# Kernel tuning notes

Measured on AMD Instinct MI355X. Metric: run time of the kernel, lower is better.

## Reference

```python
import jax, jax.numpy as jnp
import numpy as np

B, N, ND, H = 8, 1024, 64, 128
NUM_OPS, NUM_PARAMS, SKETCH = 64, 256, 128


def setup_inputs() -> dict:
    key = jax.random.key(0)
    ks = iter(jax.random.split(key, 64))

    def rn(shape, s=0.05):
        return jax.random.normal(next(ks), shape, dtype=jnp.float32) * s

    inp = {
        'node_features': jax.random.normal(next(ks), (B, N, ND), dtype=jnp.float32),
        'adjacency': (jax.random.uniform(next(ks), (B, N, N)) < 0.05).astype(jnp.float32),
        'mask': jnp.ones((B, N), jnp.float32),
    }
    for name, din in (('g1', ND), ('g2', H), ('g3', H)):
        inp[name + '_W'] = rn((din, H))
        inp[name + '_b'] = jnp.zeros((H,), jnp.float32)
        inp[name + '_aW'] = rn((2 * H,))
        inp[name + '_ab'] = jnp.zeros((), jnp.float32)
    for l in (0, 1):
        inp[f'l{l}_Wih'] = rn((4 * H, H))
        inp[f'l{l}_Whh'] = rn((4 * H, H))
        inp[f'l{l}_bih'] = jnp.zeros((4 * H,), jnp.float32)
        inp[f'l{l}_bhh'] = jnp.zeros((4 * H,), jnp.float32)
    for name, dout in (('op', NUM_OPS), ('pa', NUM_PARAMS), ('sk', SKETCH), ('no', ND)):
        inp[name + '_W1'] = rn((H, H))
        inp[name + '_b1'] = jnp.zeros((H,), jnp.float32)
        inp[name + '_W2'] = rn((H, dout))
        inp[name + '_b2'] = jnp.zeros((dout,), jnp.float32)
    return inp


def _gnn(x, adj, W, b, aW, ab):
    # h = Linear(x); att[b,i,j] = sigmoid(aW . [h_j ; h_i] + ab)  (cat order from the torch code)
    h = x @ W + b                      # [B,N,H]
    D = W.shape[1]
    sj = h @ aW[:D]                    # contribution of the dim-1-expanded term (h_j)
    si = h @ aW[D:]                    # contribution of the dim-2-expanded term (h_i)
    att = jax.nn.sigmoid(si[:, :, None] + sj[:, None, :] + ab) * adj  # [B,N,N]
    return jnp.einsum('bij,bjd->bid', att, h)


def _lstm(x, Wih, Whh, bih, bhh):
    # single torch-style LSTM layer, gate order i,f,g,o; zero initial state
    Bx, Hh = x.shape[0], Whh.shape[1]

    def step(carry, xt):
        h, c = carry
        g = xt @ Wih.T + h @ Whh.T + (bih + bhh)       # [B,4H]
        i, f, gg, o = jnp.split(g, 4, axis=-1)
        c = jax.nn.sigmoid(f) * c + jax.nn.sigmoid(i) * jnp.tanh(gg)
        h = jax.nn.sigmoid(o) * jnp.tanh(c)
        return (h, c), h

    z = jnp.zeros((Bx, Hh), x.dtype)
    _, ys = jax.lax.scan(step, (z, z), jnp.swapaxes(x, 0, 1))
    return jnp.swapaxes(ys, 0, 1)


def _mlp(x, W1, b1, W2, b2):
    return jax.nn.relu(x @ W1 + b1) @ W2 + b2


def reference(node_features, adjacency, mask,
              g1_W, g1_b, g1_aW, g1_ab,
              g2_W, g2_b, g2_aW, g2_ab,
              g3_W, g3_b, g3_aW, g3_ab,
              l0_Wih, l0_Whh, l0_bih, l0_bhh,
              l1_Wih, l1_Whh, l1_bih, l1_bhh,
              op_W1, op_b1, op_W2, op_b2,
              pa_W1, pa_b1, pa_W2, pa_b2,
              sk_W1, sk_b1, sk_W2, sk_b2,
              no_W1, no_b1, no_W2, no_b2):
    h = jax.nn.relu(_gnn(node_features, adjacency, g1_W, g1_b, g1_aW, g1_ab))
    h = jax.nn.relu(_gnn(h, adjacency, g2_W, g2_b, g2_aW, g2_ab))
    h = _gnn(h, adjacency, g3_W, g3_b, g3_aW, g3_ab)
    lo = _lstm(h, l0_Wih, l0_Whh, l0_bih, l0_bhh)
    lo = _lstm(lo, l1_Wih, l1_Whh, l1_bih, l1_bhh)
    op_pred = _mlp(lo, op_W1, op_b1, op_W2, op_b2)
    param_pred = _mlp(lo, pa_W1, pa_b1, pa_W2, pa_b2)
    sketch_pred = _mlp(lo, sk_W1, sk_b1, sk_W2, sk_b2)
    node_pred = _mlp(h, no_W1, no_b1, no_W2, no_b2)
    return (op_pred, param_pred, sketch_pred, node_pred)
```

## Files before the change

### kernel.cpp

```cpp
#include <hip/hip_runtime.h>
#include <hip/hip_fp16.h>

typedef __attribute__((ext_vector_type(8))) short short8;
typedef __attribute__((ext_vector_type(4))) float f32x4;
typedef __attribute__((ext_vector_type(2))) unsigned int u32x2;

__device__ __forceinline__ unsigned short bf16_of(float f) {
    unsigned u = __builtin_bit_cast(unsigned, f);
    u += 0x7fffu + ((u >> 16) & 1u);
    return (unsigned short)(u >> 16);
}
__device__ __forceinline__ unsigned bf16pk(float a, float b) {
    return (unsigned)bf16_of(a) | ((unsigned)bf16_of(b) << 16);
}
__device__ __forceinline__ unsigned fp16pk(float a, float b) {
    return __builtin_bit_cast(unsigned, __builtin_amdgcn_cvt_pkrtz(a, b));
}
__device__ __forceinline__ f32x4 h4f(u32x2 v) {
    __half2 a = __builtin_bit_cast(__half2, v[0]);
    __half2 b = __builtin_bit_cast(__half2, v[1]);
    float2 fa = __half22float2(a), fb = __half22float2(b);
    f32x4 r; r[0] = fa.x; r[1] = fa.y; r[2] = fb.x; r[3] = fb.y;
    return r;
}
__device__ __forceinline__ float fexp2(float x) { return __builtin_amdgcn_exp2f(x); }
__device__ __forceinline__ float frcp(float x) { return __builtin_amdgcn_rcpf(x); }
__device__ __forceinline__ float sigm(float x) { return frcp(1.f + fexp2(-1.44269504f * x)); }
__device__ __forceinline__ f32x4 mfma16(short8 a, short8 b, f32x4 c) {
    return __builtin_amdgcn_mfma_f32_16x16x32_bf16(a, b, c, 0, 0, 0);
}
__device__ __forceinline__ float dpp_shr8(float x) {
    return __builtin_bit_cast(float, __builtin_amdgcn_update_dpp(
        0, __builtin_bit_cast(int, x), 0x118, 0xF, 0xF, true));
}
__device__ __forceinline__ float dpp_shl8(float x) {
    return __builtin_bit_cast(float, __builtin_amdgcn_update_dpp(
        0, __builtin_bit_cast(int, x), 0x108, 0xF, 0xF, true));
}

struct PrepArgs {
    const float* src[8];
    unsigned short* dst[8];
    int N[8];
};

__global__ __launch_bounds__(256) void gemm_f32(
    const float* __restrict__ A, const float* __restrict__ B,
    const float* __restrict__ bias, float* __restrict__ C,
    int M, int N, int K, int BT, int RELU, int PACK)
{
    __shared__ float As[64][33];
    __shared__ float Bs[32][68];
    const int tid = threadIdx.x;
    const int tx = tid & 15, ty = tid >> 4;
    const int m0 = blockIdx.y * 64, n0 = blockIdx.x * 64;
    float acc[4][4];
#pragma unroll
    for (int i = 0; i < 4; ++i)
#pragma unroll
        for (int j = 0; j < 4; ++j) acc[i][j] = 0.f;

    for (int k0 = 0; k0 < K; k0 += 32) {
        __syncthreads();
        {
            const int r = tid >> 2, kk = (tid & 3) * 8;
            const float* src = A + (size_t)(m0 + r) * K + k0 + kk;
            f32x4 v0 = *(const f32x4*)src;
            f32x4 v1 = *(const f32x4*)(src + 4);
#pragma unroll
            for (int e = 0; e < 4; ++e) { As[r][kk + e] = v0[e]; As[r][kk + 4 + e] = v1[e]; }
        }
        if (!BT) {
            const int kk = tid >> 3, nn = (tid & 7) * 8;
            const float* src = B + (size_t)(k0 + kk) * N + n0 + nn;
            f32x4 v0 = *(const f32x4*)src;
            f32x4 v1 = *(const f32x4*)(src + 4);
#pragma unroll
            for (int e = 0; e < 4; ++e) { Bs[kk][nn + e] = v0[e]; Bs[kk][nn + 4 + e] = v1[e]; }
        } else {
            const int n = tid >> 2, kk = (tid & 3) * 8;
            const float* src = B + (size_t)(n0 + n) * K + k0 + kk;
            f32x4 v0 = *(const f32x4*)src;
            f32x4 v1 = *(const f32x4*)(src + 4);
#pragma unroll
            for (int e = 0; e < 4; ++e) { Bs[kk + e][n] = v0[e]; Bs[kk + 4 + e][n] = v1[e]; }
        }
        __syncthreads();
#pragma unroll 8
        for (int k = 0; k < 32; ++k) {
            float a0 = As[ty * 4 + 0][k], a1 = As[ty * 4 + 1][k];
            float a2 = As[ty * 4 + 2][k], a3 = As[ty * 4 + 3][k];
            f32x4 bv = *(const f32x4*)&Bs[k][tx * 4];
#pragma unroll
            for (int j = 0; j < 4; ++j) {
                acc[0][j] += a0 * bv[j]; acc[1][j] += a1 * bv[j];
                acc[2][j] += a2 * bv[j]; acc[3][j] += a3 * bv[j];
            }
        }
    }
    f32x4 bv = {};
    if (bias != nullptr) bv = *(const f32x4*)&bias[n0 + tx * 4];
#pragma unroll
    for (int i = 0; i < 4; ++i) {
        f32x4 res = {};
#pragma unroll
        for (int j = 0; j < 4; ++j) {
            float v = acc[i][j] + bv[j];
            if (RELU) v = fmaxf(v, 0.f);
            res[j] = v;
        }
        const int m = m0 + ty * 4 + i;
        if (!PACK) {
            *(f32x4*)&C[(size_t)m * N + n0 + tx * 4] = res;
        } else {
            const int b = m >> 10, t = m & 1023;
            const int n = n0 + tx * 4;
            const int pr = n >> 7, h = n & 127;
            if (pr == 3) {
#pragma unroll
                for (int j = 0; j < 4; ++j) res[j] *= 0.5f;
            }
            __half* Ch = (__half*)C;
            u32x2 ov = {fp16pk(res[0], res[1]), fp16pk(res[2], res[3])};
            *(u32x2*)&Ch[(((size_t)t * 4 + pr) * 8 + b) * 128 + h] = ov;
        }
    }
}

__global__ __launch_bounds__(256) void gemm_gnn(
    const float* __restrict__ A, const float* __restrict__ B,
    const float* __restrict__ bias, const float* __restrict__ aW,
    unsigned short* __restrict__ hT, float* __restrict__ siP,
    float* __restrict__ sjP, int K,
    PrepArgs pa, const float* __restrict__ bih0, const float* __restrict__ bhh0,
    float* __restrict__ bsum, int* __restrict__ flags)
{
    const int tid = threadIdx.x;
    if (blockIdx.y >= 256) {
        const int pid = (blockIdx.y - 256) * 2 + blockIdx.x;
        if (pid < 8) {
            const float* src = pa.src[pid];
            unsigned short* dst = pa.dst[pid];
            const int N = pa.N[pid];
            const int n0 = tid >> 4, kc = (tid & 15) * 8;
            for (int n = n0; n < N; n += 16) {
                unsigned o[4];
#pragma unroll
                for (int e = 0; e < 8; e += 2)
                    o[e >> 1] = bf16pk(src[(size_t)(kc + e) * N + n],
                                       src[(size_t)(kc + e + 1) * N + n]);
                *(u32x2*)&dst[n * 128 + kc] = *(u32x2*)&o[0];
                *(u32x2*)&dst[n * 128 + kc + 4] = *(u32x2*)&o[2];
            }
        } else if (pid == 8) {
            bsum[tid] = bih0[tid] + bhh0[tid];
            bsum[tid + 256] = bih0[tid + 256] + bhh0[tid + 256];
            if (tid < 3) flags[tid] = 0;
        }
        return;
    }

    __shared__ float As[32][33];
    __shared__ float Bs[32][68];
    __shared__ unsigned short T[32][70];
    const int tx = tid & 15, ty = tid >> 4;
    const int m0 = blockIdx.y * 32, n0 = blockIdx.x * 64;
    float acc[2][4];
#pragma unroll
    for (int i = 0; i < 2; ++i)
#pragma unroll
        for (int j = 0; j < 4; ++j) acc[i][j] = 0.f;

    for (int k0 = 0; k0 < K; k0 += 32) {
        __syncthreads();
        {
            const int r = tid >> 3, kk = (tid & 7) * 4;
            f32x4 v = *(const f32x4*)(A + (size_t)(m0 + r) * K + k0 + kk);
#pragma unroll
            for (int e = 0; e < 4; ++e) As[r][kk + e] = v[e];
        }
        {
            const int kk = tid >> 3, nn = (tid & 7) * 8;
            const float* src = B + (size_t)(k0 + kk) * 128 + n0 + nn;
            f32x4 v0 = *(const f32x4*)src;
            f32x4 v1 = *(const f32x4*)(src + 4);
#pragma unroll
            for (int e = 0; e < 4; ++e) { Bs[kk][nn + e] = v0[e]; Bs[kk][nn + 4 + e] = v1[e]; }
        }
        __syncthreads();
#pragma unroll 8
        for (int k = 0; k < 32; ++k) {
            float a0 = As[ty * 2 + 0][k], a1 = As[ty * 2 + 1][k];
            f32x4 bv = *(const f32x4*)&Bs[k][tx * 4];
#pragma unroll
            for (int j = 0; j < 4; ++j) {
                acc[0][j] += a0 * bv[j];
                acc[1][j] += a1 * bv[j];
            }
        }
    }
    f32x4 bv = *(const f32x4*)&bias[n0 + tx * 4];
#pragma unroll
    for (int i = 0; i < 2; ++i)
#pragma unroll
        for (int j = 0; j < 4; ++j) acc[i][j] += bv[j];

    f32x4 wj = *(const f32x4*)&aW[n0 + tx * 4];
    f32x4 wi = *(const f32x4*)&aW[128 + n0 + tx * 4];
#pragma unroll
    for (int i = 0; i < 2; ++i) {
        float pj = acc[i][0] * wj[0] + acc[i][1] * wj[1] + acc[i][2] * wj[2] + acc[i][3] * wj[3];
        float pi = acc[i][0] * wi[0] + acc[i][1] * wi[1] + acc[i][2] * wi[2] + acc[i][3] * wi[3];
#pragma unroll
        for (int o = 8; o > 0; o >>= 1) {
            pj += __shfl_xor(pj, o);
            pi += __shfl_xor(pi, o);
        }
        if (tx == 0) {
            const int m = m0 + ty * 2 + i;
            sjP[blockIdx.x * 8192 + m] = pj;
            siP[blockIdx.x * 8192 + m] = pi;
        }
    }

#pragma unroll
    for (int i = 0; i < 2; ++i) {
        unsigned* tp = (unsigned*)&T[ty * 2 + i][tx * 4];
        tp[0] = bf16pk(acc[i][0], acc[i][1]);
        tp[1] = bf16pk(acc[i][2], acc[i][3]);
    }
    __syncthreads();
    const int b = m0 >> 10, node0 = m0 & 1023;
    const int dr = tid >> 4, npair = tid & 15;
#pragma unroll
    for (int rr = 0; rr < 4; ++rr) {
        const int d = rr * 16 + dr;
        unsigned o = (unsigned)T[npair * 2][d] | ((unsigned)T[npair * 2 + 1][d] << 16);
        *(unsigned*)(hT + ((size_t)b * 128 + n0 + d) * 1024 + node0 + npair * 2) = o;
    }
}

__global__ __launch_bounds__(256) void gnn_agg(
    const float* __restrict__ adj, const unsigned short* __restrict__ hT,
    const float* __restrict__ siP, const float* __restrict__ sjP,
    const float* __restrict__ abp, float* __restrict__ out, int RELU)
{
    __shared__ __align__(16) unsigned short Alds[32 * 40];
    __shared__ __align__(16) unsigned short Blds[128 * 40];
    __shared__ float sjL[1024];
    const int b = blockIdx.y, it = blockIdx.x;
    const int i0 = it * 32;
    const int tid = threadIdx.x, lane = tid & 63, w = tid >> 6;
    const int quad = lane >> 4, col = lane & 15;
    const int rh = w & 1, nh = w >> 1;
    const float ab = abp[0];
    const float* adjb = adj + (size_t)b * 1024 * 1024;
    const unsigned short* hTb = hT + (size_t)b * 128 * 1024;

    for (int j = tid; j < 1024; j += 256)
        sjL[j] = sjP[b * 1024 + j] + sjP[8192 + b * 1024 + j];

    const int ar_ = tid >> 3, ash = (tid & 7) * 4;
    const int br_ = tid >> 1, bsh = (tid & 1) * 16;
    const float sii = siP[b * 1024 + i0 + ar_] + siP[8192 + b * 1024 + i0 + ar_] + ab;

    const float* aptr = adjb + (size_t)(i0 + ar_) * 1024 + ash;
    const unsigned short* bptr = hTb + (size_t)br_ * 1024 + bsh;

    f32x4 paA = *(const f32x4*)(aptr);
    short8 pbA0 = *(const short8*)(bptr);
    short8 pbA1 = *(const short8*)(bptr + 8);
    f32x4 paB = *(const f32x4*)(aptr + 32);
    short8 pbB0 = *(const short8*)(bptr + 32);
    short8 pbB1 = *(const short8*)(bptr + 40);

    f32x4 acc[4] = {};

    for (int j0 = 0; j0 < 1024; j0 += 64) {
        __syncthreads();
        {
            float s0 = sigm(sii + sjL[j0 + ash + 0]) * paA[0];
            float s1 = sigm(sii + sjL[j0 + ash + 1]) * paA[1];
            float s2 = sigm(sii + sjL[j0 + ash + 2]) * paA[2];
            float s3 = sigm(sii + sjL[j0 + ash + 3]) * paA[3];
            u32x2 o = {bf16pk(s0, s1), bf16pk(s2, s3)};
            *(u32x2*)&Alds[ar_ * 40 + ash] = o;
            *(short8*)&Blds[br_ * 40 + bsh] = pbA0;
            *(short8*)&Blds[br_ * 40 + bsh + 8] = pbA1;
        }
        if (j0 + 64 < 1024) {
            paA = *(const f32x4*)(aptr + j0 + 64);
            pbA0 = *(const short8*)(bptr + j0 + 64);
            pbA1 = *(const short8*)(bptr + j0 + 72);
        }
        __syncthreads();
        {
            short8 af = *(const short8*)&Alds[(rh * 16 + col) * 40 + quad * 8];
#pragma unroll
            for (int nt = 0; nt < 4; ++nt) {
                short8 bf = *(const short8*)&Blds[((nh * 4 + nt) * 16 + col) * 40 + quad * 8];
                acc[nt] = mfma16(af, bf, acc[nt]);
            }
        }
        __syncthreads();
        {
            float s0 = sigm(sii + sjL[j0 + 32 + ash + 0]) * paB[0];
            float s1 = sigm(sii + sjL[j0 + 32 + ash + 1]) * paB[1];
            float s2 = sigm(sii + sjL[j0 + 32 + ash + 2]) * paB[2];
            float s3 = sigm(sii + sjL[j0 + 32 + ash + 3]) * paB[3];
            u32x2 o = {bf16pk(s0, s1), bf16pk(s2, s3)};
            *(u32x2*)&Alds[ar_ * 40 + ash] = o;
            *(short8*)&Blds[br_ * 40 + bsh] = pbB0;
            *(short8*)&Blds[br_ * 40 + bsh + 8] = pbB1;
        }
        if (j0 + 96 < 1024) {
            paB = *(const f32x4*)(aptr + j0 + 96);
            pbB0 = *(const short8*)(bptr + j0 + 96);
            pbB1 = *(const short8*)(bptr + j0 + 104);
        }
        __syncthreads();
        {
            short8 af = *(const short8*)&Alds[(rh * 16 + col) * 40 + quad * 8];
#pragma unroll
            for (int nt = 0; nt < 4; ++nt) {
                short8 bf = *(const short8*)&Blds[((nh * 4 + nt) * 16 + col) * 40 + quad * 8];
                acc[nt] = mfma16(af, bf, acc[nt]);
            }
        }
    }
    const int ibase = i0 + rh * 16 + quad * 4;
#pragma unroll
    for (int nt = 0; nt < 4; ++nt) {
        const int d = (nh * 4 + nt) * 16 + col;
#pragma unroll
        for (int r = 0; r < 4; ++r) {
            float v = acc[nt][r];
            if (RELU) v = fmaxf(v, 0.f);
            out[((size_t)b * 1024 + ibase + r) * 128 + d] = v;
        }
    }
}


struct HeadArgs {
    const unsigned short* W1T[4];
    const float* b1[4];
    const unsigned short* W2T[4];
    const float* b2[4];
    float* outp[4];
};

__device__ __forceinline__ void lstm_epilogue(
    const f32x4 accs[4], f32x4 xv0, f32x4 xv1, float* cst, float* hv,
    bool lo, float selLo)
{
    float t0[4], t1[4];
#pragma unroll
    for (int i = 0; i < 4; ++i) {
        float P0 = (lo ? accs[0][i] : dpp_shr8(accs[1][i])) + xv0[i];
        float P1 = (lo ? accs[2][i] : dpp_shr8(accs[3][i])) + xv1[i];
        P1 = fmaxf(P1, -30.f);
        t0[i] = frcp(1.f + fexp2(-1.44269504f * P0));
        float u = fexp2(-2.88539008f * P1);
        t1[i] = (1.f - selLo * u) * frcp(1.f + u);
    }
    float c2[4], og[4];
#pragma unroll
    for (int i = 0; i < 4; ++i) {
        float ig = t0[i];
        float fg = dpp_shl8(t0[i]);
        float gg = t1[i];
        og[i] = dpp_shl8(t1[i]);
        c2[i] = fg * cst[i] + ig * gg;
        cst[i] = c2[i];
    }
    float pc0 = lo ? c2[0] : dpp_shr8(c2[1]);
    float pc1 = lo ? c2[2] : dpp_shr8(c2[3]);
    pc0 = fmaxf(pc0, -30.f);
    pc1 = fmaxf(pc1, -30.f);
    float u0 = fexp2(-2.88539008f * pc0);
    float tc0 = (1.f - u0) * frcp(1.f + u0);
    float u1 = fexp2(-2.88539008f * pc1);
    float tc1 = (1.f - u1) * frcp(1.f + u1);
    float th[4] = {tc0, dpp_shl8(tc0), tc1, dpp_shl8(tc1)};
#pragma unroll
    for (int i = 0; i < 4; ++i) hv[i] = og[i] * th[i];
}

template <int SINK>
__device__ __forceinline__ void lstm_step(
    unsigned short* Hc, unsigned short* Hn, const short8 afr[4][4],
    f32x4 xv0, f32x4 xv1, float* cst, unsigned short* __restrict__ sink,
    int t, int col, int quad, int h4, int b)
{
    short8 bfr[4];
#pragma unroll
    for (int c = 0; c < 4; ++c)
        bfr[c] = *(const short8*)&Hc[col * 136 + c * 32 + quad * 8];
    f32x4 accs[4] = {};
#pragma unroll
    for (int c = 0; c < 4; ++c)
#pragma unroll
        for (int g = 0; g < 4; ++g)
            accs[g] = mfma16(afr[g][c], bfr[c], accs[g]);

    const bool lo = (col < 8);
    const float selLo = lo ? 1.f : 0.f;
    float hv[4];
    lstm_epilogue(accs, xv0, xv1, cst, hv, lo, selLo);
    if (lo) {
        u32x2 hb = {bf16pk(hv[0], hv[1]), bf16pk(hv[2], hv[3])};
        *(u32x2*)&Hn[b * 136 + h4] = hb;
        if (SINK == 0)
            *(u32x2*)(sink + (size_t)t * 1024 + b * 128 + h4) = hb;
        else
            *(u32x2*)(sink + ((size_t)t * 8 + b) * 128 + h4) = hb;
    }
    __builtin_amdgcn_s_waitcnt(0xC07F);
    __builtin_amdgcn_s_barrier();
}

template <int A32, int LROWS>
__device__ void head_strip(
    const void* __restrict__ Asrc, int row0,
    const unsigned short* __restrict__ W1T, const float* __restrict__ b1,
    const unsigned short* __restrict__ W2T, const float* __restrict__ b2,
    float* __restrict__ outp, int dout, unsigned short* A2, int tid)
{
    const int lane = tid & 63, w = tid >> 6;
    const int quad = lane >> 4, col = lane & 15;
    const int mrow = w * 16 + col;
    f32x4 acc[8] = {};
#pragma unroll
    for (int kc = 0; kc < 4; ++kc) {
        short8 af;
        if (A32) {
            const float* s = (const float*)Asrc + (size_t)(row0 + mrow) * 128 + kc * 32 + quad * 8;
            f32x4 v0 = *(const f32x4*)s, v1 = *(const f32x4*)(s + 4);
            short8 v;
#pragma unroll
            for (int j = 0; j < 4; ++j) {
                v[j] = (short)bf16_of(v0[j]);
                v[4 + j] = (short)bf16_of(v1[j]);
            }
            af = v;
        } else {
            af = *(const short8*)((const unsigned short*)Asrc +
                                  (size_t)(row0 + mrow) * 128 + kc * 32 + quad * 8);
        }
#pragma unroll
        for (int nt = 0; nt < 8; ++nt) {
            short8 bf = *(const short8*)&W1T[(nt * 16 + col) * 128 + kc * 32 + quad * 8];
            acc[nt] = mfma16(af, bf, acc[nt]);
        }
    }
    float b1v[8];
#pragma unroll
    for (int nt = 0; nt < 8; ++nt) b1v[nt] = b1[nt * 16 + col];
    __syncthreads();
#pragma unroll
    for (int nt = 0; nt < 8; ++nt)
#pragma unroll
        for (int i = 0; i < 4; ++i) {
            const int mm = w * 16 + quad * 4 + i;
            A2[mm * 136 + nt * 16 + col] = bf16_of(fmaxf(acc[nt][i] + b1v[nt], 0.f));
        }
    __syncthreads();
    const int ntiles = dout >> 4;
    for (int np = 0; np < ntiles; np += 8) {
        const int nts = (ntiles - np < 8) ? ntiles - np : 8;
        f32x4 acc2[8] = {};
#pragma unroll
        for (int kc = 0; kc < 4; ++kc) {
            short8 a2f = *(const short8*)&A2[mrow * 136 + kc * 32 + quad * 8];
            for (int nt = 0; nt < nts; ++nt) {
                short8 bf = *(const short8*)&W2T[((np + nt) * 16 + col) * 128 + kc * 32 + quad * 8];
                acc2[nt] = mfma16(a2f, bf, acc2[nt]);
            }
        }
        for (int nt = 0; nt < nts; ++nt) {
            const int n = (np + nt) * 16 + col;
            const float bb = b2[n];
#pragma unroll
            for (int i = 0; i < 4; ++i) {
                const int r = row0 + w * 16 + quad * 4 + i;
                size_t off;
                if (LROWS) off = ((size_t)(r & 7) * 1024 + (r >> 3)) * dout + n;
                else       off = (size_t)r * dout + n;
                outp[off] = acc2[nt][i] + bb;
            }
        }
    }
}

__global__ __launch_bounds__(512, 2) void lstm_pipe(
    const __half* __restrict__ xw0, const float* __restrict__ Whh0,
    const float* __restrict__ Wih1, const float* __restrict__ Whh1,
    const float* __restrict__ bih1, const float* __restrict__ bhh1,
    unsigned short* __restrict__ hbuf, __half* __restrict__ xw1,
    int* __restrict__ flags, unsigned short* __restrict__ out1b,
    const float* __restrict__ bufH3, HeadArgs ha)
{
    __shared__ __align__(16) unsigned short H[2][16 * 136];
    __shared__ __align__(16) unsigned short A2[128 * 136];
    const int tid = threadIdx.x;
    const int lane = tid & 63;
    const int w = tid >> 6;
    const int quad = lane >> 4;
    const int col = lane & 15;
    const int b = col & 7;
    const int prA = col >> 3;
    const int h4 = w * 16 + quad * 4;

    if (blockIdx.x >= 3) {
        const int wid = blockIdx.x - 3;
        for (int s = wid; s < 64; s += 8)
            head_strip<1, 0>(bufH3, s * 128, ha.W1T[3], ha.b1[3],
                             ha.W2T[3], ha.b2[3], ha.outp[3], 64, A2, tid);
        for (int s = wid; s < 64; s += 8) {
            if (tid == 0) {
                while (__hip_atomic_load(&flags[2], __ATOMIC_ACQUIRE,
                                         __HIP_MEMORY_SCOPE_AGENT) < s + 1)
                    __builtin_amdgcn_s_sleep(16);
            }
            __syncthreads();
            head_strip<0, 1>(out1b, s * 128, ha.W1T[0], ha.b1[0],
                             ha.W2T[0], ha.b2[0], ha.outp[0], 64, A2, tid);
            head_strip<0, 1>(out1b, s * 128, ha.W1T[1], ha.b1[1],
                             ha.W2T[1], ha.b2[1], ha.outp[1], 256, A2, tid);
            head_strip<0, 1>(out1b, s * 128, ha.W1T[2], ha.b1[2],
                             ha.W2T[2], ha.b2[2], ha.outp[2], 128, A2, tid);
        }
        return;
    }

    if (blockIdx.x == 1) {
        short8 afrI[4][4];
        f32x4 biasv[4];
#pragma unroll
        for (int g = 0; g < 4; ++g) {
            const float gsc = (g == 3) ? 0.5f : 1.f;
            const int row = g * 128 + w * 16 + col;
#pragma unroll
            for (int c = 0; c < 4; ++c) {
                const float* src = Wih1 + row * 128 + c * 32 + quad * 8;
                short8 v;
#pragma unroll
                for (int j = 0; j < 8; ++j) v[j] = (short)bf16_of(src[j] * gsc);
                afrI[g][c] = v;
            }
            const int rb = g * 128 + w * 16 + quad * 4;
            f32x4 b1 = *(const f32x4*)&bih1[rb];
            f32x4 b2 = *(const f32x4*)&bhh1[rb];
#pragma unroll
            for (int e = 0; e < 4; ++e) biasv[g][e] = (b1[e] + b2[e]) * gsc;
        }
        for (int k = 0; k < 64; ++k) {
            if (tid == 0) {
                while (__hip_atomic_load(&flags[0], __ATOMIC_ACQUIRE,
                                         __HIP_MEMORY_SCOPE_AGENT) < k + 1)
                    __builtin_amdgcn_s_sleep(2);
                if (k >= 4) {
                    while (__hip_atomic_load(&flags[2], __ATOMIC_RELAXED,
                                             __HIP_MEMORY_SCOPE_AGENT) < k - 3)
                        __builtin_amdgcn_s_sleep(2);
                }
            }
            __builtin_amdgcn_s_waitcnt(0xC07F);
            __builtin_amdgcn_s_barrier();
            const unsigned short* hb = hbuf + (size_t)k * 16 * 1024;
            __half* dst = xw1 + (size_t)(k & 3) * 65536;
#pragma unroll 2
            for (int nt = 0; nt < 8; ++nt) {
                const int tl = nt * 2 + (col >> 3);
                const unsigned short* src = hb + tl * 1024 + b * 128 + quad * 8;
                short8 bfr[4];
#pragma unroll
                for (int c = 0; c < 4; ++c) bfr[c] = *(const short8*)&src[c * 32];
                f32x4 acc[4] = {};
#pragma unroll
                for (int c = 0; c < 4; ++c)
#pragma unroll
                    for (int g = 0; g < 4; ++g)
                        acc[g] = mfma16(afrI[g][c], bfr[c], acc[g]);
#pragma unroll
                for (int g = 0; g < 4; ++g) {
                    u32x2 res = {fp16pk(acc[g][0] + biasv[g][0], acc[g][1] + biasv[g][1]),
                                 fp16pk(acc[g][2] + biasv[g][2], acc[g][3] + biasv[g][3])};
                    *(u32x2*)&dst[((tl * 4 + g) * 8 + b) * 128 + w * 16 + quad * 4] = res;
                }
            }
            __builtin_amdgcn_s_waitcnt(0x0F70);
            __builtin_amdgcn_s_barrier();
            if (tid == 0)
                __hip_atomic_store(&flags[1], k + 1, __ATOMIC_RELEASE,
                                   __HIP_MEMORY_SCOPE_AGENT);
        }
        return;
    }

    for (int i = tid; i < 2 * 16 * 136; i += 512) (&H[0][0])[i] = 0;
    float cst[4] = {0.f, 0.f, 0.f, 0.f};
    const int lane_off = (prA * 8 + b) * 128 + h4;

    if (blockIdx.x == 0) {
        short8 afr[4][4];
#pragma unroll
        for (int g = 0; g < 4; ++g) {
            const float gsc = (g == 3) ? 0.5f : 1.f;
            const int row = g * 128 + w * 16 + col;
#pragma unroll
            for (int c = 0; c < 4; ++c) {
                const float* src = Whh0 + row * 128 + c * 32 + quad * 8;
                short8 v;
#pragma unroll
                for (int j = 0; j < 8; ++j) v[j] = (short)bf16_of(src[j] * gsc);
                afr[g][c] = v;
            }
        }
        const __half* xp = xw0 + lane_off;
        u32x2 p0a = *(const u32x2*)(xp);
        u32x2 p1a = *(const u32x2*)(xp + 2048);
        u32x2 p0b = *(const u32x2*)(xp + 4096);
        u32x2 p1b = *(const u32x2*)(xp + 6144);
        xp += 8192;
        __syncthreads();

        for (int t = 0; t < 1024; t += 2) {
            const __half* xr = (t == 1022) ? xp - 8192 : xp;
            {
                f32x4 xv0 = h4f(p0a), xv1 = h4f(p1a);
                p0a = *(const u32x2*)(xr);
                p1a = *(const u32x2*)(xr + 2048);
                lstm_step<0>(&H[0][0], &H[1][0], afr, xv0, xv1, cst, hbuf, t, col, quad, h4, b);
            }
            {
                f32x4 xv0 = h4f(p0b), xv1 = h4f(p1b);
                p0b = *(const u32x2*)(xr + 4096);
                p1b = *(const u32x2*)(xr + 6144);
                lstm_step<0>(&H[1][0], &H[0][0], afr, xv0, xv1, cst, hbuf, t + 1, col, quad, h4, b);
            }
            xp += 8192;
            if ((t & 14) == 14) {
                __syncthreads();
                if (tid == 0)
                    __hip_atomic_store(&flags[0], (t >> 4) + 1, __ATOMIC_RELEASE,
                                       __HIP_MEMORY_SCOPE_AGENT);
            }
        }
    } else {
        short8 afr[4][4];
#pragma unroll
        for (int g = 0; g < 4; ++g) {
            const float gsc = (g == 3) ? 0.5f : 1.f;
            const int row = g * 128 + w * 16 + col;
#pragma unroll
            for (int c = 0; c < 4; ++c) {
                const float* src = Whh1 + row * 128 + c * 32 + quad * 8;
                short8 v;
#pragma unroll
                for (int j = 0; j < 8; ++j) v[j] = (short)bf16_of(src[j] * gsc);
                afr[g][c] = v;
            }
        }
        __syncthreads();
        auto xaddr = [&](int t) -> const __half* {
            return xw1 + (((t >> 4) & 3) * 65536 + (t & 15) * 4096) + lane_off;
        };
        while (__hip_atomic_load(&flags[1], __ATOMIC_ACQUIRE,
                                 __HIP_MEMORY_SCOPE_AGENT) < 2)
            __builtin_amdgcn_s_sleep(2);
        u32x2 p0a = *(const u32x2*)xaddr(0);
        u32x2 p1a = *(const u32x2*)(xaddr(0) + 2048);
        u32x2 p0b = *(const u32x2*)xaddr(1);
        u32x2 p1b = *(const u32x2*)(xaddr(1) + 2048);

        for (int c = 0; c < 64; ++c) {
            if (c > 0) {
                const int target = (c + 2 < 64) ? c + 2 : 64;
                if (tid == 0) {
                    while (__hip_atomic_load(&flags[1], __ATOMIC_ACQUIRE,
                                             __HIP_MEMORY_SCOPE_AGENT) < target)
                        __builtin_amdgcn_s_sleep(2);
                }
                __builtin_amdgcn_s_waitcnt(0xC07F);
                __builtin_amdgcn_s_barrier();
            }
            for (int s = 0; s < 16; s += 2) {
                const int t = c * 16 + s;
                const int t2 = (t + 2 < 1024) ? t + 2 : 1023;
                const int t3 = (t + 3 < 1024) ? t + 3 : 1023;
                {
                    f32x4 xv0 = h4f(p0a), xv1 = h4f(p1a);
                    p0a = *(const u32x2*)xaddr(t2);
                    p1a = *(const u32x2*)(xaddr(t2) + 2048);
                    lstm_step<1>(&H[0][0], &H[1][0], afr, xv0, xv1, cst, out1b, t, col, quad, h4, b);
                }
                {
                    f32x4 xv0 = h4f(p0b), xv1 = h4f(p1b);
                    p0b = *(const u32x2*)xaddr(t3);
                    p1b = *(const u32x2*)(xaddr(t3) + 2048);
                    lstm_step<1>(&H[1][0], &H[0][0], afr, xv0, xv1, cst, out1b, t + 1, col, quad, h4, b);
                }
            }
            __syncthreads();
            if (tid == 0)
                __hip_atomic_store(&flags[2], c + 1, __ATOMIC_RELEASE,
                                   __HIP_MEMORY_SCOPE_AGENT);
        }
    }
}

extern "C" void kernel_launch(void* const* d_in, const int* in_sizes, int n_in,
                              void* d_out, int out_size, void* d_ws, size_t ws_size,
                              hipStream_t stream)
{
    (void)in_sizes; (void)n_in; (void)out_size; (void)ws_size;
    const float* nf    = (const float*)d_in[0];
    const float* adj   = (const float*)d_in[1];
    const float* g1W   = (const float*)d_in[3];
    const float* g1b   = (const float*)d_in[4];
    const float* g1aW  = (const float*)d_in[5];
    const float* g1ab  = (const float*)d_in[6];
    const float* g2W   = (const float*)d_in[7];
    const float* g2b   = (const float*)d_in[8];
    const float* g2aW  = (const float*)d_in[9];
    const float* g2ab  = (const float*)d_in[10];
    const float* g3W   = (const float*)d_in[11];
    const float* g3b   = (const float*)d_in[12];
    const float* g3aW  = (const float*)d_in[13];
    const float* g3ab  = (const float*)d_in[14];
    const float* l0Wih = (const float*)d_in[15];
    const float* l0Whh = (const float*)d_in[16];
    const float* l0bih = (const float*)d_in[17];
    const float* l0bhh = (const float*)d_in[18];
    const float* l1Wih = (const float*)d_in[19];
    const float* l1Whh = (const float*)d_in[20];
    const float* l1bih = (const float*)d_in[21];
    const float* l1bhh = (const float*)d_in[22];
    const float* opW1 = (const float*)d_in[23];
    const float* opb1 = (const float*)d_in[24];
    const float* opW2 = (const float*)d_in[25];
    const float* opb2 = (const float*)d_in[26];
    const float* paW1 = (const float*)d_in[27];
    const float* pab1 = (const float*)d_in[28];
    const float* paW2 = (const float*)d_in[29];
    const float* pab2 = (const float*)d_in[30];
    const float* skW1 = (const float*)d_in[31];
    const float* skb1 = (const float*)d_in[32];
    const float* skW2 = (const float*)d_in[33];
    const float* skb2 = (const float*)d_in[34];
    const float* noW1 = (const float*)d_in[35];
    const float* nob1 = (const float*)d_in[36];
    const float* noW2 = (const float*)d_in[37];
    const float* nob2 = (const float*)d_in[38];

    float* out = (float*)d_out;
    float* ws = (float*)d_ws;
    float* siP   = ws;
    float* sjP   = ws + 16384;
    float* bufX  = ws + 1048576;
    float* bufH3 = ws + 2097152;
    unsigned short* bufT = (unsigned short*)(ws + 3145728);
    float* bsum = ws + 3686400;
    float* xw0f = ws + 3687424;
    float* xw1f = ws + 7881728;
    int*  flags = (int*)(ws + 8143872);
    unsigned short* WT = (unsigned short*)(ws + 8143876);
    unsigned short* out1b = (unsigned short*)(ws + 8209412);
    unsigned short* hbuf = (unsigned short*)bufX;
    __half* xw0 = (__half*)xw0f;
    __half* xw1 = (__half*)xw1f;

    unsigned short* opW1T = WT;
    unsigned short* paW1T = WT + 16384;
    unsigned short* skW1T = WT + 32768;
    unsigned short* noW1T = WT + 49152;
    unsigned short* opW2T = WT + 65536;
    unsigned short* paW2T = WT + 73728;
    unsigned short* skW2T = WT + 106496;
    unsigned short* noW2T = WT + 122880;

    PrepArgs pargs;
    pargs.src[0] = opW1; pargs.dst[0] = opW1T; pargs.N[0] = 128;
    pargs.src[1] = paW1; pargs.dst[1] = paW1T; pargs.N[1] = 128;
    pargs.src[2] = skW1; pargs.dst[2] = skW1T; pargs.N[2] = 128;
    pargs.src[3] = noW1; pargs.dst[3] = noW1T; pargs.N[3] = 128;
    pargs.src[4] = opW2; pargs.dst[4] = opW2T; pargs.N[4] = 64;
    pargs.src[5] = paW2; pargs.dst[5] = paW2T; pargs.N[5] = 256;
    pargs.src[6] = skW2; pargs.dst[6] = skW2T; pargs.N[6] = 128;
    pargs.src[7] = noW2; pargs.dst[7] = noW2T; pargs.N[7] = 64;

    gemm_gnn<<<dim3(2, 261), 256, 0, stream>>>(nf, g1W, g1b, g1aW, bufT, siP, sjP, 64,
                                               pargs, l0bih, l0bhh, bsum, flags);
    gnn_agg<<<dim3(32, 8), 256, 0, stream>>>(adj, bufT, siP, sjP, g1ab, bufX, 1);
    gemm_gnn<<<dim3(2, 256), 256, 0, stream>>>(bufX, g2W, g2b, g2aW, bufT, siP, sjP, 128,
                                               pargs, l0bih, l0bhh, bsum, flags);
    gnn_agg<<<dim3(32, 8), 256, 0, stream>>>(adj, bufT, siP, sjP, g2ab, bufX, 1);
    gemm_gnn<<<dim3(2, 256), 256, 0, stream>>>(bufX, g3W, g3b, g3aW, bufT, siP, sjP, 128,
                                               pargs, l0bih, l0bhh, bsum, flags);
    gnn_agg<<<dim3(32, 8), 256, 0, stream>>>(adj, bufT, siP, sjP, g3ab, bufH3, 0);

    {
        dim3 g(512 / 64, 8192 / 64);
        gemm_f32<<<g, dim3(256), 0, stream>>>(bufH3, l0Wih, bsum, (float*)xw0,
                                              8192, 512, 128, 1, 0, 1);
    }

    HeadArgs ha;
    ha.W1T[0] = opW1T; ha.b1[0] = opb1; ha.W2T[0] = opW2T; ha.b2[0] = opb2;
    ha.outp[0] = out + 0;
    ha.W1T[1] = paW1T; ha.b1[1] = pab1; ha.W2T[1] = paW2T; ha.b2[1] = pab2;
    ha.outp[1] = out + 524288;
    ha.W1T[2] = skW1T; ha.b1[2] = skb1; ha.W2T[2] = skW2T; ha.b2[2] = skb2;
    ha.outp[2] = out + 2621440;
    ha.W1T[3] = noW1T; ha.b1[3] = nob1; ha.W2T[3] = noW2T; ha.b2[3] = nob2;
    ha.outp[3] = out + 3670016;
    lstm_pipe<<<11, 512, 0, stream>>>(xw0, l0Whh, l1Wih, l1Whh, l1bih, l1bhh,
                                      hbuf, xw1, flags, out1b, bufH3, ha);
}
```

Before: 1.325 ms.

## Fuse layer-0 LSTM input projection into LSTM pipeline with flag-gated chunked producers

Removes the separate fp32 gemm_f32 launch that computed the layer-0 input projection xw0. Sixteen extra blocks in lstm_pipe now compute it with bf16 MFMA in 64-timestep chunks, signalling per-chunk flags that the recurrent block waits on before consuming each chunk. This overlaps the projection with the sequential recurrence and drops a kernel launch. The cost is extra polling and barriers inside the recurrent loop, bf16 instead of fp32 precision for the projection, and more concurrent blocks competing for the device.

```diff
diff --git a/kernel.cpp b/kernel.cpp
--- a/kernel.cpp
+++ b/kernel.cpp
@@ -44,96 +44,13 @@
     int N[8];
 };
 
-__global__ __launch_bounds__(256) void gemm_f32(
-    const float* __restrict__ A, const float* __restrict__ B,
-    const float* __restrict__ bias, float* __restrict__ C,
-    int M, int N, int K, int BT, int RELU, int PACK)
-{
-    __shared__ float As[64][33];
-    __shared__ float Bs[32][68];
-    const int tid = threadIdx.x;
-    const int tx = tid & 15, ty = tid >> 4;
-    const int m0 = blockIdx.y * 64, n0 = blockIdx.x * 64;
-    float acc[4][4];
-#pragma unroll
-    for (int i = 0; i < 4; ++i)
-#pragma unroll
-        for (int j = 0; j < 4; ++j) acc[i][j] = 0.f;
-
-    for (int k0 = 0; k0 < K; k0 += 32) {
-        __syncthreads();
-        {
-            const int r = tid >> 2, kk = (tid & 3) * 8;
-            const float* src = A + (size_t)(m0 + r) * K + k0 + kk;
-            f32x4 v0 = *(const f32x4*)src;
-            f32x4 v1 = *(const f32x4*)(src + 4);
-#pragma unroll
-            for (int e = 0; e < 4; ++e) { As[r][kk + e] = v0[e]; As[r][kk + 4 + e] = v1[e]; }
-        }
-        if (!BT) {
-            const int kk = tid >> 3, nn = (tid & 7) * 8;
-            const float* src = B + (size_t)(k0 + kk) * N + n0 + nn;
-            f32x4 v0 = *(const f32x4*)src;
-            f32x4 v1 = *(const f32x4*)(src + 4);
-#pragma unroll
-            for (int e = 0; e < 4; ++e) { Bs[kk][nn + e] = v0[e]; Bs[kk][nn + 4 + e] = v1[e]; }
-        } else {
-            const int n = tid >> 2, kk = (tid & 3) * 8;
-            const float* src = B + (size_t)(n0 + n) * K + k0 + kk;
-            f32x4 v0 = *(const f32x4*)src;
-            f32x4 v1 = *(const f32x4*)(src + 4);
-#pragma unroll
-            for (int e = 0; e < 4; ++e) { Bs[kk + e][n] = v0[e]; Bs[kk + 4 + e][n] = v1[e]; }
-        }
-        __syncthreads();
-#pragma unroll 8
-        for (int k = 0; k < 32; ++k) {
-            float a0 = As[ty * 4 + 0][k], a1 = As[ty * 4 + 1][k];
-            float a2 = As[ty * 4 + 2][k], a3 = As[ty * 4 + 3][k];
-            f32x4 bv = *(const f32x4*)&Bs[k][tx * 4];
-#pragma unroll
-            for (int j = 0; j < 4; ++j) {
-                acc[0][j] += a0 * bv[j]; acc[1][j] += a1 * bv[j];
-                acc[2][j] += a2 * bv[j]; acc[3][j] += a3 * bv[j];
-            }
-        }
-    }
-    f32x4 bv = {};
-    if (bias != nullptr) bv = *(const f32x4*)&bias[n0 + tx * 4];
-#pragma unroll
-    for (int i = 0; i < 4; ++i) {
-        f32x4 res = {};
-#pragma unroll
-        for (int j = 0; j < 4; ++j) {
-            float v = acc[i][j] + bv[j];
-            if (RELU) v = fmaxf(v, 0.f);
-            res[j] = v;
-        }
-        const int m = m0 + ty * 4 + i;
-        if (!PACK) {
-            *(f32x4*)&C[(size_t)m * N + n0 + tx * 4] = res;
-        } else {
-            const int b = m >> 10, t = m & 1023;
-            const int n = n0 + tx * 4;
-            const int pr = n >> 7, h = n & 127;
-            if (pr == 3) {
-#pragma unroll
-                for (int j = 0; j < 4; ++j) res[j] *= 0.5f;
-            }
-            __half* Ch = (__half*)C;
-            u32x2 ov = {fp16pk(res[0], res[1]), fp16pk(res[2], res[3])};
-            *(u32x2*)&Ch[(((size_t)t * 4 + pr) * 8 + b) * 128 + h] = ov;
-        }
-    }
-}
-
 __global__ __launch_bounds__(256) void gemm_gnn(
     const float* __restrict__ A, const float* __restrict__ B,
     const float* __restrict__ bias, const float* __restrict__ aW,
     unsigned short* __restrict__ hT, float* __restrict__ siP,
     float* __restrict__ sjP, int K,
-    PrepArgs pa, const float* __restrict__ bih0, const float* __restrict__ bhh0,
-    float* __restrict__ bsum, int* __restrict__ flags)
+    PrepArgs pa, const float* __restrict__ wih,
+    unsigned short* __restrict__ wihB, int* __restrict__ flags)
 {
     const int tid = threadIdx.x;
     if (blockIdx.y >= 256) {
@@ -153,9 +70,20 @@
                 *(u32x2*)&dst[n * 128 + kc + 4] = *(u32x2*)&o[2];
             }
         } else if (pid == 8) {
-            bsum[tid] = bih0[tid] + bhh0[tid];
-            bsum[tid + 256] = bih0[tid + 256] + bhh0[tid + 256];
-            if (tid < 3) flags[tid] = 0;
+            if (tid < 19) flags[tid] = 0;
+        } else if (pid < 13) {
+            const int base = (pid - 9) * 16384;
+            for (int i = tid * 8; i < 16384; i += 2048) {
+                const float* s = wih + base + i;
+                f32x4 v0 = *(const f32x4*)s, v1 = *(const f32x4*)(s + 4);
+                short8 o;
+#pragma unroll
+                for (int j = 0; j < 4; ++j) {
+                    o[j] = (short)bf16_of(v0[j]);
+                    o[4 + j] = (short)bf16_of(v1[j]);
+                }
+                *(short8*)(wihB + base + i) = o;
+            }
         }
         return;
     }
@@ -499,7 +427,9 @@
     const float* __restrict__ bih1, const float* __restrict__ bhh1,
     unsigned short* __restrict__ hbuf, __half* __restrict__ xw1,
     int* __restrict__ flags, unsigned short* __restrict__ out1b,
-    const float* __restrict__ bufH3, HeadArgs ha)
+    const float* __restrict__ bufH3, HeadArgs ha,
+    const float* __restrict__ bih0, const float* __restrict__ bhh0,
+    const unsigned short* __restrict__ WihB)
 {
     __shared__ __align__(16) unsigned short H[2][16 * 136];
     __shared__ __align__(16) unsigned short A2[128 * 136];
@@ -512,6 +442,73 @@
     const int prA = col >> 3;
     const int h4 = w * 16 + quad * 4;
 
+    if (blockIdx.x >= 11) {
+        const int wid = blockIdx.x - 11;
+        unsigned short* hA = A2;
+        const float gsc = (w >= 6) ? 0.5f : 1.f;
+        float bs[4];
+#pragma unroll
+        for (int nt = 0; nt < 4; ++nt) {
+            const int n = w * 64 + nt * 16 + col;
+            bs[nt] = bih0[n] + bhh0[n];
+        }
+        for (int idx = wid; idx < 128; idx += 16) {
+            const int g = idx >> 3, bq = idx & 7;
+            const int row0 = bq * 1024 + g * 64;
+            {
+                const int r = tid >> 3, c0 = (tid & 7) * 16;
+                const float* src = bufH3 + (size_t)(row0 + r) * 128 + c0;
+                unsigned short* dst = hA + r * 136 + c0;
+#pragma unroll
+                for (int e = 0; e < 16; e += 8) {
+                    f32x4 v0 = *(const f32x4*)(src + e);
+                    f32x4 v1 = *(const f32x4*)(src + e + 4);
+                    short8 o;
+#pragma unroll
+                    for (int j = 0; j < 4; ++j) {
+                        o[j] = (short)bf16_of(v0[j]);
+                        o[4 + j] = (short)bf16_of(v1[j]);
+                    }
+                    *(short8*)(dst + e) = o;
+                }
+            }
+            __syncthreads();
+#pragma unroll
+            for (int rt = 0; rt < 4; ++rt) {
+                short8 af[4];
+#pragma unroll
+                for (int c = 0; c < 4; ++c)
+                    af[c] = *(const short8*)&hA[(rt * 16 + col) * 136 + c * 32 + quad * 8];
+                f32x4 acc[4] = {};
+#pragma unroll
+                for (int c = 0; c < 4; ++c)
+#pragma unroll
+                    for (int nt = 0; nt < 4; ++nt) {
+                        short8 bf = *(const short8*)&WihB[(size_t)(w * 64 + nt * 16 + col) * 128 + c * 32 + quad * 8];
+                        acc[nt] = mfma16(af[c], bf, acc[nt]);
+                    }
+#pragma unroll
+                for (int nt = 0; nt < 4; ++nt) {
+                    const int pr = w >> 1;
+                    const int h = (w & 1) * 64 + nt * 16 + col;
+#pragma unroll
+                    for (int i = 0; i < 4; ++i) {
+                        const int t_ = g * 64 + rt * 16 + quad * 4 + i;
+                        __half* dst = (__half*)xw0 +
+                            (((size_t)t_ * 4 + pr) * 8 + bq) * 128 + h;
+                        *dst = (__half)((acc[nt][i] + bs[nt]) * gsc);
+                    }
+                }
+            }
+            __builtin_amdgcn_s_waitcnt(0x0F70);
+            __builtin_amdgcn_s_barrier();
+            if (tid == 0)
+                __hip_atomic_fetch_add(&flags[3 + g], 1, __ATOMIC_RELEASE,
+                                       __HIP_MEMORY_SCOPE_AGENT);
+        }
+        return;
+    }
+
     if (blockIdx.x >= 3) {
         const int wid = blockIdx.x - 3;
         for (int s = wid; s < 64; s += 8)
@@ -618,6 +615,12 @@
                 afr[g][c] = v;
             }
         }
+        if (tid == 0) {
+            while (__hip_atomic_load(&flags[3], __ATOMIC_ACQUIRE,
+                                     __HIP_MEMORY_SCOPE_AGENT) < 8)
+                __builtin_amdgcn_s_sleep(2);
+        }
+        __syncthreads();
         const __half* xp = xw0 + lane_off;
         u32x2 p0a = *(const u32x2*)(xp);
         u32x2 p1a = *(const u32x2*)(xp + 2048);
@@ -627,6 +630,18 @@
         __syncthreads();
 
         for (int t = 0; t < 1024; t += 2) {
+            if ((t & 63) == 48) {
+                const int gw = (t >> 6) + 1;
+                if (gw < 16) {
+                    if (tid == 0) {
+                        while (__hip_atomic_load(&flags[3 + gw], __ATOMIC_ACQUIRE,
+                                                 __HIP_MEMORY_SCOPE_AGENT) < 8)
+                            __builtin_amdgcn_s_sleep(2);
+                    }
+                    __builtin_amdgcn_s_waitcnt(0xC07F);
+                    __builtin_amdgcn_s_barrier();
+                }
+            }
             const __half* xr = (t == 1022) ? xp - 8192 : xp;
             {
                 f32x4 xv0 = h4f(p0a), xv1 = h4f(p1a);
@@ -759,13 +774,13 @@
     float* ws = (float*)d_ws;
     float* siP   = ws;
     float* sjP   = ws + 16384;
+    unsigned short* WihB = (unsigned short*)(ws + 40960);
     float* bufX  = ws + 1048576;
     float* bufH3 = ws + 2097152;
     unsigned short* bufT = (unsigned short*)(ws + 3145728);
-    float* bsum = ws + 3686400;
+    int*  flags = (int*)(ws + 3686400);
     float* xw0f = ws + 3687424;
     float* xw1f = ws + 7881728;
-    int*  flags = (int*)(ws + 8143872);
     unsigned short* WT = (unsigned short*)(ws + 8143876);
     unsigned short* out1b = (unsigned short*)(ws + 8209412);
     unsigned short* hbuf = (unsigned short*)bufX;
@@ -791,21 +806,15 @@
     pargs.src[6] = skW2; pargs.dst[6] = skW2T; pargs.N[6] = 128;
     pargs.src[7] = noW2; pargs.dst[7] = noW2T; pargs.N[7] = 64;
 
-    gemm_gnn<<<dim3(2, 261), 256, 0, stream>>>(nf, g1W, g1b, g1aW, bufT, siP, sjP, 64,
-                                               pargs, l0bih, l0bhh, bsum, flags);
+    gemm_gnn<<<dim3(2, 263), 256, 0, stream>>>(nf, g1W, g1b, g1aW, bufT, siP, sjP, 64,
+                                               pargs, l0Wih, WihB, flags);
     gnn_agg<<<dim3(32, 8), 256, 0, stream>>>(adj, bufT, siP, sjP, g1ab, bufX, 1);
     gemm_gnn<<<dim3(2, 256), 256, 0, stream>>>(bufX, g2W, g2b, g2aW, bufT, siP, sjP, 128,
-                                               pargs, l0bih, l0bhh, bsum, flags);
+                                               pargs, l0Wih, WihB, flags);
     gnn_agg<<<dim3(32, 8), 256, 0, stream>>>(adj, bufT, siP, sjP, g2ab, bufX, 1);
     gemm_gnn<<<dim3(2, 256), 256, 0, stream>>>(bufX, g3W, g3b, g3aW, bufT, siP, sjP, 128,
-                                               pargs, l0bih, l0bhh, bsum, flags);
+                                               pargs, l0Wih, WihB, flags);
     gnn_agg<<<dim3(32, 8), 256, 0, stream>>>(adj, bufT, siP, sjP, g3ab, bufH3, 0);
-
-    {
-        dim3 g(512 / 64, 8192 / 64);
-        gemm_f32<<<g, dim3(256), 0, stream>>>(bufH3, l0Wih, bsum, (float*)xw0,
-                                              8192, 512, 128, 1, 0, 1);
-    }
 
     HeadArgs ha;
     ha.W1T[0] = opW1T; ha.b1[0] = opb1; ha.W2T[0] = opW2T; ha.b2[0] = opb2;
@@ -816,6 +825,7 @@
     ha.outp[2] = out + 2621440;
     ha.W1T[3] = noW1T; ha.b1[3] = nob1; ha.W2T[3] = noW2T; ha.b2[3] = nob2;
     ha.outp[3] = out + 3670016;
-    lstm_pipe<<<11, 512, 0, stream>>>(xw0, l0Whh, l1Wih, l1Whh, l1bih, l1bhh,
-                                      hbuf, xw1, flags, out1b, bufH3, ha);
-}
+    lstm_pipe<<<27, 512, 0, stream>>>(xw0, l0Whh, l1Wih, l1Whh, l1bih, l1bhh,
+                                      hbuf, xw1, flags, out1b, bufH3, ha,
+                                      l0bih, l0bhh, WihB);
+}
```

New measurement: 1.310 ms, median of 2. Within noise of the previous version (-1.1%).
